# Performance work log

Hardware: AMD Instinct MI355X
Metric: run time of the kernel (lower is better)

## Reference

```python
import jax, jax.numpy as jnp
import numpy as np

B, T, I, H, O = 64, 1024, 512, 1024, 512


def setup_inputs() -> dict:
    key = jax.random.key(0)
    ks = jax.random.split(key, 8)
    s_in = 1.0 / np.sqrt(I)
    s_g = 1.0 / np.sqrt(2 * H)
    s_o = 1.0 / np.sqrt(H)
    return {
        "inputs": jax.random.normal(ks[0], (B, T, I), dtype=jnp.float32),
        "h": jax.random.normal(ks[1], (B, H), dtype=jnp.float32),
        "W_in": jax.random.uniform(ks[2], (H, I), minval=-s_in, maxval=s_in, dtype=jnp.float32),
        "b_in": jax.random.uniform(ks[3], (H,), minval=-s_in, maxval=s_in, dtype=jnp.float32),
        "W_gate": jax.random.uniform(ks[4], (H, 2 * H), minval=-s_g, maxval=s_g, dtype=jnp.float32),
        "b_gate": jax.random.uniform(ks[5], (H,), minval=-s_g, maxval=s_g, dtype=jnp.float32),
        "W_out": jax.random.uniform(ks[6], (O, H), minval=-s_o, maxval=s_o, dtype=jnp.float32),
        "b_out": jax.random.uniform(ks[7], (O,), minval=-s_o, maxval=s_o, dtype=jnp.float32),
    }


def reference(inputs, h, W_in, b_in, W_gate, b_gate, W_out, b_out):
    # input_layer has no time dependence -> compute for all steps at once.
    # z: [T, B, H]
    z = jnp.einsum("bti,hi->tbh", inputs, W_in) + b_in
    # gate_layer acts on cat([h, z_t]); split its weight accordingly.
    Wg_h = W_gate[:, :H]   # [H, H] applied to h
    Wg_z = W_gate[:, H:]   # [H, H] applied to z_t

    def step(h_prev, z_t):
        u = jax.nn.sigmoid(h_prev @ Wg_h.T + z_t @ Wg_z.T + b_gate)
        h_new = u * h_prev + (1.0 - u) * z_t
        return h_new, h_new

    h_final, hs = jax.lax.scan(step, h, z)  # hs: [T, B, H]
    # output_layer applied to every hidden state, vectorized over time.
    outs = jnp.einsum("tbh,oh->bto", hs, W_out) + b_out  # [B, T, O]
    return (outs, h_final)
```

## Files before the change

### kernel.cpp

```cpp
#include <hip/hip_runtime.h>

#define B_ 64
#define T_ 1024
#define I_ 512
#define H_ 1024
#define O_ 512
#define BH (B_*H_)

using short8 = __attribute__((ext_vector_type(8))) short;
using f32x4  = __attribute__((ext_vector_type(4))) float;

__device__ __forceinline__ unsigned short f2b(float f) {
  unsigned int u = __float_as_uint(f);
  u = (u + 0x7fffu + ((u >> 16) & 1u)) >> 16;
  return (unsigned short)u;
}
__device__ __forceinline__ float b2f(unsigned short h) {
  return __uint_as_float(((unsigned int)h) << 16);
}

#define WAIT_VM0() __builtin_amdgcn_s_waitcnt(0x0F70)

__global__ void cast4_kernel(const float* __restrict__ src, ushort* __restrict__ dst, int n4) {
  int i = blockIdx.x * 256 + threadIdx.x;
  if (i >= n4) return;
  float4 v = ((const float4*)src)[i];
  ushort4 o; o.x = f2b(v.x); o.y = f2b(v.y); o.z = f2b(v.z); o.w = f2b(v.w);
  ((ushort4*)dst)[i] = o;
}

__global__ void cast_gate_kernel(const float* __restrict__ src, ushort* __restrict__ dst) {
  int i = blockIdx.x * 256 + threadIdx.x;
  int row = i >> 8, k4 = (i & 255) << 2;
  float4 v = *(const float4*)(src + (size_t)row * 2048 + 1024 + k4);
  ushort4 o; o.x = f2b(v.x); o.y = f2b(v.y); o.z = f2b(v.z); o.w = f2b(v.w);
  ((ushort4*)dst)[((size_t)row << 8) + (k4 >> 2)] = o;
}

__global__ __launch_bounds__(256)
void gemm_bt(const void* __restrict__ A, const ushort* __restrict__ W,
             const float* __restrict__ bias, void* __restrict__ Cout,
             int M, int N, int K, int modeA, int modeC)
{
  int wave = threadIdx.x >> 6, lane = threadIdx.x & 63;
  int q = lane >> 4, col = lane & 15;
  int r0 = blockIdx.y * 64 + wave * 16;
  int n0 = blockIdx.x * 64;
  int arow = r0 + col;

  const ushort* Ab = nullptr;
  const float*  Af = nullptr;
  if (modeA == 0) {
    Ab = (const ushort*)A + (size_t)arow * K + q * 8;
  } else {
    int b = arow & 63, t = arow >> 6;
    Af = (const float*)A + ((size_t)b * T_ + t) * (size_t)K + q * 8;
  }
  const ushort* Wp = W + (size_t)(n0 + col) * K + q * 8;

  f32x4 acc[4];
  #pragma unroll
  for (int nt = 0; nt < 4; ++nt) acc[nt] = (f32x4){0.f, 0.f, 0.f, 0.f};

  if (modeA == 0) {
    for (int k0 = 0; k0 < K; k0 += 32) {
      short8 af = *(const short8*)(Ab + k0);
      #pragma unroll
      for (int nt = 0; nt < 4; ++nt) {
        short8 bf_ = *(const short8*)(Wp + (size_t)nt * 16 * K + k0);
        acc[nt] = __builtin_amdgcn_mfma_f32_16x16x32_bf16(af, bf_, acc[nt], 0, 0, 0);
      }
    }
  } else {
    for (int k0 = 0; k0 < K; k0 += 32) {
      float4 f0 = *(const float4*)(Af + k0);
      float4 f1 = *(const float4*)(Af + k0 + 4);
      short8 af;
      af[0] = (short)f2b(f0.x); af[1] = (short)f2b(f0.y);
      af[2] = (short)f2b(f0.z); af[3] = (short)f2b(f0.w);
      af[4] = (short)f2b(f1.x); af[5] = (short)f2b(f1.y);
      af[6] = (short)f2b(f1.z); af[7] = (short)f2b(f1.w);
      #pragma unroll
      for (int nt = 0; nt < 4; ++nt) {
        short8 bf_ = *(const short8*)(Wp + (size_t)nt * 16 * K + k0);
        acc[nt] = __builtin_amdgcn_mfma_f32_16x16x32_bf16(af, bf_, acc[nt], 0, 0, 0);
      }
    }
  }

  #pragma unroll
  for (int nt = 0; nt < 4; ++nt) {
    int n = n0 + nt * 16 + col;
    float bv = bias[n];
    #pragma unroll
    for (int r = 0; r < 4; ++r) {
      int row = r0 + q * 4 + r;
      float v = acc[nt][r] + bv;
      if (modeC == 0) {
        ((ushort*)Cout)[(size_t)row * N + n] = f2b(v);
      } else {
        int b = row & 63, t = row >> 6;
        ((float*)Cout)[(size_t)b * (T_ * O_) + (size_t)t * O_ + n] = v;
      }
    }
  }
}

__device__ __forceinline__ void scan_step(
    int t, int g, int b0, int n0, int lane, int q, int col,
    const short8* __restrict__ wfv, ushort* __restrict__ hbuf,
    float* __restrict__ hfinal, int* __restrict__ flags,
    const float zv[4], const float av[4], float hp[4])
{
  const int fidx = (g << 6) + lane;
  for (;;) {
    int v = __hip_atomic_load(&flags[fidx], __ATOMIC_RELAXED, __HIP_MEMORY_SCOPE_AGENT);
    if (__ballot(v < t) == 0ull) break;
    __builtin_amdgcn_s_sleep(1);
  }
  __builtin_amdgcn_fence(__ATOMIC_ACQUIRE, "workgroup");

  const ushort* hrow = hbuf + (size_t)(t - 1) * BH + (size_t)(b0 + col) * H_ + q * 8;
  f32x4 acc0 = {0.f, 0.f, 0.f, 0.f}, acc1 = {0.f, 0.f, 0.f, 0.f};
  #pragma unroll
  for (int ks = 0; ks < 32; ks += 2) {
    short8 h0f = *(const short8*)(hrow + ks * 32);
    short8 h1f = *(const short8*)(hrow + (ks + 1) * 32);
    acc0 = __builtin_amdgcn_mfma_f32_16x16x32_bf16(h0f, wfv[ks * 64 + lane], acc0, 0, 0, 0);
    acc1 = __builtin_amdgcn_mfma_f32_16x16x32_bf16(h1f, wfv[(ks + 1) * 64 + lane], acc1, 0, 0, 0);
  }
  f32x4 S = acc0 + acc1;

  #pragma unroll
  for (int r = 0; r < 4; ++r) {
    int b = b0 + q * 4 + r;
    float x  = S[r] + av[r];
    float u  = 1.0f / (1.0f + __expf(-x));
    float hn = u * hp[r] + (1.0f - u) * zv[r];
    hp[r] = hn;
    unsigned int own = f2b(hn);
    unsigned int other = ((unsigned int)__shfl_xor((int)own, 1, 64)) & 0xffffu;
    if ((col & 1) == 0) {
      unsigned int dw = own | (other << 16);
      __hip_atomic_store((unsigned int*)(hbuf + (size_t)t * BH + (size_t)b * H_ + n0 + col),
                         dw, __ATOMIC_RELAXED, __HIP_MEMORY_SCOPE_AGENT);
    }
    if (t == T_) hfinal[(size_t)b * H_ + n0 + col] = hn;
  }
  WAIT_VM0();
  if (lane == 0)
    __hip_atomic_store(&flags[(g << 6) + (n0 >> 4)], t + 1,
                       __ATOMIC_RELAXED, __HIP_MEMORY_SCOPE_AGENT);
}

__global__ __launch_bounds__(64)
void scan_kernel(const ushort* __restrict__ z, const ushort* __restrict__ a,
                 ushort* __restrict__ hbuf, const float* __restrict__ Wgate,
                 const float* __restrict__ h0, float* __restrict__ hfinal,
                 int* __restrict__ flags)
{
  __shared__ __align__(16) short Wf[32 * 64 * 8];

  const int tid = threadIdx.x;
  const int member = blockIdx.x & 63;
  const int pairid = blockIdx.x >> 6;
  const int gA = pairid * 2, gB = pairid * 2 + 1;
  const int b0A = gA << 4, b0B = gB << 4;
  const int n0 = member << 4;
  const int lane = tid;
  const int q = lane >> 4, col = lane & 15;

  short8* wfv = (short8*)Wf;

  {
    const float* wsrc = Wgate + (size_t)(n0 + col) * 2048 + (q * 8);
    for (int ks = 0; ks < 32; ++ks) {
      float4 w0 = *(const float4*)(wsrc + ks * 32);
      float4 w1 = *(const float4*)(wsrc + ks * 32 + 4);
      short8 v;
      v[0] = (short)f2b(w0.x); v[1] = (short)f2b(w0.y);
      v[2] = (short)f2b(w0.z); v[3] = (short)f2b(w0.w);
      v[4] = (short)f2b(w1.x); v[5] = (short)f2b(w1.y);
      v[6] = (short)f2b(w1.z); v[7] = (short)f2b(w1.w);
      wfv[ks * 64 + lane] = v;
    }
  }

  #pragma unroll
  for (int grp = 0; grp < 2; ++grp) {
    int b0 = grp ? b0B : b0A;
    #pragma unroll
    for (int i = 0; i < 2; ++i) {
      int idx = tid + 64 * i;
      int b = b0 + (idx >> 3);
      int n = n0 + (idx & 7) * 2;
      const float* hp0 = h0 + (size_t)b * H_ + n;
      unsigned int dw = (unsigned int)f2b(hp0[0]) | ((unsigned int)f2b(hp0[1]) << 16);
      __hip_atomic_store((unsigned int*)(hbuf + (size_t)b * H_ + n), dw,
                         __ATOMIC_RELAXED, __HIP_MEMORY_SCOPE_AGENT);
    }
  }

  float hpA[4], hpB[4];
  #pragma unroll
  for (int r = 0; r < 4; ++r) {
    hpA[r] = h0[(size_t)(b0A + q * 4 + r) * H_ + n0 + col];
    hpB[r] = h0[(size_t)(b0B + q * 4 + r) * H_ + n0 + col];
  }

  WAIT_VM0();
  if (tid == 0) {
    __hip_atomic_store(&flags[(gA << 6) + member], 1, __ATOMIC_RELAXED, __HIP_MEMORY_SCOPE_AGENT);
    __hip_atomic_store(&flags[(gB << 6) + member], 1, __ATOMIC_RELAXED, __HIP_MEMORY_SCOPE_AGENT);
  }

  for (int t = 1; t <= T_; ++t) {
    float zvA[4], avA[4], zvB[4], avB[4];
    {
      const size_t baseA = (size_t)(t - 1) * BH + (size_t)(b0A + q * 4) * H_ + n0 + col;
      const size_t baseB = (size_t)(t - 1) * BH + (size_t)(b0B + q * 4) * H_ + n0 + col;
      #pragma unroll
      for (int r = 0; r < 4; ++r) {
        zvA[r] = b2f(z[baseA + (size_t)r * H_]);
        avA[r] = b2f(a[baseA + (size_t)r * H_]);
        zvB[r] = b2f(z[baseB + (size_t)r * H_]);
        avB[r] = b2f(a[baseB + (size_t)r * H_]);
      }
    }
    scan_step(t, gA, b0A, n0, lane, q, col, wfv, hbuf, hfinal, flags, zvA, avA, hpA);
    scan_step(t, gB, b0B, n0, lane, q, col, wfv, hbuf, hfinal, flags, zvB, avB, hpB);
  }
}

extern "C" void kernel_launch(void* const* d_in, const int* in_sizes, int n_in,
                              void* d_out, int out_size, void* d_ws, size_t ws_size,
                              hipStream_t stream) {
  const float* inputs = (const float*)d_in[0];
  const float* h0     = (const float*)d_in[1];
  const float* W_in   = (const float*)d_in[2];
  const float* b_in   = (const float*)d_in[3];
  const float* W_gate = (const float*)d_in[4];
  const float* b_gate = (const float*)d_in[5];
  const float* W_out  = (const float*)d_in[6];
  const float* b_out  = (const float*)d_in[7];

  char* ws = (char*)d_ws;
  ushort* Winbf  = (ushort*)(ws + 0);
  ushort* Wgzbf  = (ushort*)(ws + (1u << 20));
  ushort* Woutbf = (ushort*)(ws + 3 * (1u << 20));
  ushort* z_bf   = (ushort*)(ws + 4 * (1u << 20));
  ushort* a_bf   = (ushort*)(ws + (size_t)4 * (1u << 20) + (size_t)134217728);
  ushort* hbuf   = (ushort*)(ws + (size_t)4 * (1u << 20) + (size_t)2 * 134217728);
  int*    flags  = (int*)   (ws + (size_t)4 * (1u << 20) + (size_t)2 * 134217728 + (size_t)134348800);

  hipMemsetAsync(flags, 0, 4 * 64 * sizeof(int), stream);

  cast4_kernel<<<dim3((H_ * I_ / 4 + 255) / 256), dim3(256), 0, stream>>>(W_in, Winbf, H_ * I_ / 4);
  cast4_kernel<<<dim3((O_ * H_ / 4 + 255) / 256), dim3(256), 0, stream>>>(W_out, Woutbf, O_ * H_ / 4);
  cast_gate_kernel<<<dim3(H_ * H_ / 4 / 256), dim3(256), 0, stream>>>(W_gate, Wgzbf);

  gemm_bt<<<dim3(H_ / 64, (B_ * T_) / 64), dim3(256), 0, stream>>>(
      (const void*)inputs, Winbf, b_in, (void*)z_bf, B_ * T_, H_, I_, 2, 0);

  gemm_bt<<<dim3(H_ / 64, (B_ * T_) / 64), dim3(256), 0, stream>>>(
      (const void*)z_bf, Wgzbf, b_gate, (void*)a_bf, B_ * T_, H_, H_, 0, 0);

  {
    float* hfinal = (float*)d_out + (size_t)B_ * T_ * O_;
    const ushort* zc = z_bf; const ushort* ac = a_bf;
    ushort* hb = hbuf; const float* wg = W_gate; const float* h0c = h0;
    int* flg = flags;
    void* sargs[7] = { (void*)&zc, (void*)&ac, (void*)&hb, (void*)&wg,
                       (void*)&h0c, (void*)&hfinal, (void*)&flg };
    hipLaunchCooperativeKernel((const void*)scan_kernel, dim3(128), dim3(64), sargs, 0, stream);
  }

  gemm_bt<<<dim3(O_ / 64, (B_ * T_) / 64), dim3(256), 0, stream>>>(
      (const void*)(hbuf + BH), Woutbf, b_out, d_out, B_ * T_, O_, H_, 0, 1);
}
```

Baseline: 10.30 ms.

## Replace direct-load GEMMs with LDS-tiled 128x128 MFMA GEMM and pre-cast inputs

Replaces the register-only GEMM, which streamed A and W fragments straight from global memory, with a 128x128 block-tiled GEMM. It stages 32-wide K slices into LDS with global_load_lds, and each wave computes a 64x64 sub-tile of 4x4 MFMA accumulators. This raises data reuse per global load. The fp32 inputs are now cast and transposed to bf16 in time-major order in a separate kernel, with a_bf reused as the staging buffer before the gate GEMM overwrites it. The K loop has no double buffering, so loads and MFMAs still serialize behind two barriers per iteration, and the extra cast pass adds memory traffic.

```diff
diff --git a/kernel.cpp b/kernel.cpp
--- a/kernel.cpp
+++ b/kernel.cpp
@@ -21,6 +21,12 @@
 
 #define WAIT_VM0() __builtin_amdgcn_s_waitcnt(0x0F70)
 
+__device__ __forceinline__ void glds16(const ushort* g, ushort* l) {
+  __builtin_amdgcn_global_load_lds(
+      (const __attribute__((address_space(1))) void*)g,
+      (__attribute__((address_space(3))) void*)l, 16, 0, 0);
+}
+
 __global__ void cast4_kernel(const float* __restrict__ src, ushort* __restrict__ dst, int n4) {
   int i = blockIdx.x * 256 + threadIdx.x;
   if (i >= n4) return;
@@ -38,69 +44,86 @@
 }
 
 __global__ __launch_bounds__(256)
-void gemm_bt(const void* __restrict__ A, const ushort* __restrict__ W,
-             const float* __restrict__ bias, void* __restrict__ Cout,
-             int M, int N, int K, int modeA, int modeC)
+void cast_inputs_kernel(const float* __restrict__ src, ushort* __restrict__ dst) {
+  int i = blockIdx.x * 256 + threadIdx.x;
+  int rp = i >> 7;
+  int e4 = (i & 127) << 2;
+  int b = rp >> 10, t = rp & 1023;
+  float4 v = *(const float4*)(src + ((size_t)rp << 9) + e4);
+  ushort4 o; o.x = f2b(v.x); o.y = f2b(v.y); o.z = f2b(v.z); o.w = f2b(v.w);
+  *(ushort4*)(dst + (((size_t)(t << 6) + b) << 9) + e4) = o;
+}
+
+__global__ __launch_bounds__(256)
+void gemm_bt_tiled(const ushort* __restrict__ A, const ushort* __restrict__ W,
+                   const float* __restrict__ bias, void* __restrict__ Cout,
+                   int M, int N, int K, int modeC)
 {
-  int wave = threadIdx.x >> 6, lane = threadIdx.x & 63;
-  int q = lane >> 4, col = lane & 15;
-  int r0 = blockIdx.y * 64 + wave * 16;
-  int n0 = blockIdx.x * 64;
-  int arow = r0 + col;
-
-  const ushort* Ab = nullptr;
-  const float*  Af = nullptr;
-  if (modeA == 0) {
-    Ab = (const ushort*)A + (size_t)arow * K + q * 8;
-  } else {
-    int b = arow & 63, t = arow >> 6;
-    Af = (const float*)A + ((size_t)b * T_ + t) * (size_t)K + q * 8;
-  }
-  const ushort* Wp = W + (size_t)(n0 + col) * K + q * 8;
-
-  f32x4 acc[4];
-  #pragma unroll
-  for (int nt = 0; nt < 4; ++nt) acc[nt] = (f32x4){0.f, 0.f, 0.f, 0.f};
-
-  if (modeA == 0) {
-    for (int k0 = 0; k0 < K; k0 += 32) {
-      short8 af = *(const short8*)(Ab + k0);
+  __shared__ __align__(16) ushort As[128 * 32];
+  __shared__ __align__(16) ushort Bs[128 * 32];
+
+  const int tid  = threadIdx.x;
+  const int wave = tid >> 6, lane = tid & 63;
+  const int q = lane >> 4, col = lane & 15;
+
+  const int n0 = blockIdx.x * 128;
+  const int m0 = blockIdx.y * 128;
+
+  const int wr = (wave >> 1) * 64;
+  const int wc = (wave & 1) * 64;
+
+  const int srow = tid >> 2;
+  const int skk  = (tid & 3) << 3;
+  const ushort* Ag = A + (size_t)(m0 + srow) * K + skk;
+  const ushort* Wg = W + (size_t)(n0 + srow) * K + skk;
+  ushort* AsW = As + wave * 512;
+  ushort* BsW = Bs + wave * 512;
+
+  f32x4 acc[4][4];
+  #pragma unroll
+  for (int i = 0; i < 4; ++i)
+    #pragma unroll
+    for (int j = 0; j < 4; ++j) acc[i][j] = (f32x4){0.f, 0.f, 0.f, 0.f};
+
+  const ushort* Asr = As + ((size_t)(wr + col) << 5) + q * 8;
+  const ushort* Bsr = Bs + ((size_t)(wc + col) << 5) + q * 8;
+
+  for (int k0 = 0; k0 < K; k0 += 32) {
+    __syncthreads();
+    glds16(Ag + k0,                   AsW);
+    glds16(Ag + (size_t)64 * K + k0,  AsW + 2048);
+    glds16(Wg + k0,                   BsW);
+    glds16(Wg + (size_t)64 * K + k0,  BsW + 2048);
+    __syncthreads();
+
+    short8 af[4], bf[4];
+    #pragma unroll
+    for (int mt = 0; mt < 4; ++mt) af[mt] = *(const short8*)(Asr + mt * 16 * 32);
+    #pragma unroll
+    for (int nt = 0; nt < 4; ++nt) bf[nt] = *(const short8*)(Bsr + nt * 16 * 32);
+    #pragma unroll
+    for (int mt = 0; mt < 4; ++mt)
       #pragma unroll
-      for (int nt = 0; nt < 4; ++nt) {
-        short8 bf_ = *(const short8*)(Wp + (size_t)nt * 16 * K + k0);
-        acc[nt] = __builtin_amdgcn_mfma_f32_16x16x32_bf16(af, bf_, acc[nt], 0, 0, 0);
-      }
-    }
-  } else {
-    for (int k0 = 0; k0 < K; k0 += 32) {
-      float4 f0 = *(const float4*)(Af + k0);
-      float4 f1 = *(const float4*)(Af + k0 + 4);
-      short8 af;
-      af[0] = (short)f2b(f0.x); af[1] = (short)f2b(f0.y);
-      af[2] = (short)f2b(f0.z); af[3] = (short)f2b(f0.w);
-      af[4] = (short)f2b(f1.x); af[5] = (short)f2b(f1.y);
-      af[6] = (short)f2b(f1.z); af[7] = (short)f2b(f1.w);
+      for (int nt = 0; nt < 4; ++nt)
+        acc[mt][nt] = __builtin_amdgcn_mfma_f32_16x16x32_bf16(af[mt], bf[nt], acc[mt][nt], 0, 0, 0);
+  }
+
+  #pragma unroll
+  for (int nt = 0; nt < 4; ++nt) {
+    int n = n0 + wc + nt * 16 + col;
+    float bv = bias[n];
+    #pragma unroll
+    for (int mt = 0; mt < 4; ++mt) {
       #pragma unroll
-      for (int nt = 0; nt < 4; ++nt) {
-        short8 bf_ = *(const short8*)(Wp + (size_t)nt * 16 * K + k0);
-        acc[nt] = __builtin_amdgcn_mfma_f32_16x16x32_bf16(af, bf_, acc[nt], 0, 0, 0);
-      }
-    }
-  }
-
-  #pragma unroll
-  for (int nt = 0; nt < 4; ++nt) {
-    int n = n0 + nt * 16 + col;
-    float bv = bias[n];
-    #pragma unroll
-    for (int r = 0; r < 4; ++r) {
-      int row = r0 + q * 4 + r;
-      float v = acc[nt][r] + bv;
-      if (modeC == 0) {
-        ((ushort*)Cout)[(size_t)row * N + n] = f2b(v);
-      } else {
-        int b = row & 63, t = row >> 6;
-        ((float*)Cout)[(size_t)b * (T_ * O_) + (size_t)t * O_ + n] = v;
+      for (int r = 0; r < 4; ++r) {
+        int row = m0 + wr + mt * 16 + q * 4 + r;
+        float v = acc[mt][nt][r] + bv;
+        if (modeC == 0) {
+          ((ushort*)Cout)[(size_t)row * N + n] = f2b(v);
+        } else {
+          int b = row & 63, t = row >> 6;
+          ((float*)Cout)[(size_t)b * (T_ * O_) + (size_t)t * O_ + n] = v;
+        }
       }
     }
   }
@@ -253,17 +276,20 @@
   ushort* hbuf   = (ushort*)(ws + (size_t)4 * (1u << 20) + (size_t)2 * 134217728);
   int*    flags  = (int*)   (ws + (size_t)4 * (1u << 20) + (size_t)2 * 134217728 + (size_t)134348800);
 
+  ushort* Abf = a_bf;
+
   hipMemsetAsync(flags, 0, 4 * 64 * sizeof(int), stream);
 
   cast4_kernel<<<dim3((H_ * I_ / 4 + 255) / 256), dim3(256), 0, stream>>>(W_in, Winbf, H_ * I_ / 4);
   cast4_kernel<<<dim3((O_ * H_ / 4 + 255) / 256), dim3(256), 0, stream>>>(W_out, Woutbf, O_ * H_ / 4);
   cast_gate_kernel<<<dim3(H_ * H_ / 4 / 256), dim3(256), 0, stream>>>(W_gate, Wgzbf);
-
-  gemm_bt<<<dim3(H_ / 64, (B_ * T_) / 64), dim3(256), 0, stream>>>(
-      (const void*)inputs, Winbf, b_in, (void*)z_bf, B_ * T_, H_, I_, 2, 0);
-
-  gemm_bt<<<dim3(H_ / 64, (B_ * T_) / 64), dim3(256), 0, stream>>>(
-      (const void*)z_bf, Wgzbf, b_gate, (void*)a_bf, B_ * T_, H_, H_, 0, 0);
+  cast_inputs_kernel<<<dim3(B_ * T_ * I_ / 4 / 256), dim3(256), 0, stream>>>(inputs, Abf);
+
+  gemm_bt_tiled<<<dim3(H_ / 128, (B_ * T_) / 128), dim3(256), 0, stream>>>(
+      Abf, Winbf, b_in, (void*)z_bf, B_ * T_, H_, I_, 0);
+
+  gemm_bt_tiled<<<dim3(H_ / 128, (B_ * T_) / 128), dim3(256), 0, stream>>>(
+      z_bf, Wgzbf, b_gate, (void*)a_bf, B_ * T_, H_, H_, 0);
 
   {
     float* hfinal = (float*)d_out + (size_t)B_ * T_ * O_;
@@ -275,6 +301,6 @@
     hipLaunchCooperativeKernel((const void*)scan_kernel, dim3(128), dim3(64), sargs, 0, stream);
   }
 
-  gemm_bt<<<dim3(O_ / 64, (B_ * T_) / 64), dim3(256), 0, stream>>>(
-      (const void*)(hbuf + BH), Woutbf, b_out, d_out, B_ * T_, O_, H_, 0, 1);
-}
+  gemm_bt_tiled<<<dim3(O_ / 128, (B_ * T_) / 128), dim3(256), 0, stream>>>(
+      hbuf + BH, Woutbf, b_out, d_out, B_ * T_, O_, H_, 1);
+}
```

After: 8.404 ms. 18.4% less time.
